# Optimization experiments

Measured on AMD Instinct MI355X. Metric: run time of the kernel, lower is better.

The kernel has to match this reference:

```python
import jax, jax.numpy as jnp
from jax import lax
import numpy as np

BN_EPS = 1e-5


def _dwconv3x3(x, w):
    # x: [B,C,H,W], w: [C,1,3,3] depthwise (groups == C)
    return lax.conv_general_dilated(
        x, w, window_strides=(1, 1), padding='SAME',
        dimension_numbers=('NCHW', 'OIHW', 'NCHW'),
        feature_group_count=x.shape[1])


def _bn_eval(x, g, b, m, v):
    s = g * lax.rsqrt(v + BN_EPS)            # [C]
    return x * s[None, :, None, None] + (b - m * s)[None, :, None, None]


def _maxpool2(x):
    return lax.reduce_window(x, -jnp.inf, lax.max,
                             (1, 1, 2, 2), (1, 1, 2, 2), 'VALID')


def setup_inputs() -> dict:
    key = jax.random.key(0)
    ks = jax.random.split(key, 8)
    B, Cin, H, W = 32, 128, 64, 64
    Hd = 256               # hidden_size
    K, Ck = 32, 8          # num categories, hidden_size // K
    sc = 0.05
    return {
        'v4_features': jax.random.normal(ks[0], (B, Cin, H, W), jnp.float32),
        'w1_dw': jax.random.normal(ks[1], (Cin, 1, 3, 3), jnp.float32) * sc,
        'w1_pw': jax.random.normal(ks[2], (Hd, Cin), jnp.float32) * sc,
        'bn1_g': jnp.ones((Hd,), jnp.float32),
        'bn1_b': jnp.zeros((Hd,), jnp.float32),
        'bn1_m': jnp.zeros((Hd,), jnp.float32),
        'bn1_v': jnp.ones((Hd,), jnp.float32),
        'w2_dw': jax.random.normal(ks[3], (Hd, 1, 3, 3), jnp.float32) * sc,
        'w2_pw': jax.random.normal(ks[4], (Hd, Hd), jnp.float32) * sc,
        'bn2_g': jnp.ones((Hd,), jnp.float32),
        'bn2_b': jnp.zeros((Hd,), jnp.float32),
        'bn2_m': jnp.zeros((Hd,), jnp.float32),
        'bn2_v': jnp.ones((Hd,), jnp.float32),
        'cat_w': jax.random.normal(ks[5], (K, Ck, Hd), jnp.float32) * sc,
        'emb_w': jax.random.normal(ks[6], (128, Hd), jnp.float32) * sc,
        'emb_b': jnp.zeros((128,), jnp.float32),
    }


def reference(v4_features, w1_dw, w1_pw, bn1_g, bn1_b, bn1_m, bn1_v,
              w2_dw, w2_pw, bn2_g, bn2_b, bn2_m, bn2_v,
              cat_w, emb_w, emb_b):
    # Block 1: depthwise 3x3 -> pointwise 1x1 -> BN -> ReLU -> maxpool2
    x = _dwconv3x3(v4_features, w1_dw)
    x = jnp.einsum('bchw,oc->bohw', x, w1_pw)
    x = _maxpool2(jax.nn.relu(_bn_eval(x, bn1_g, bn1_b, bn1_m, bn1_v)))
    # Block 2
    x = _dwconv3x3(x, w2_dw)
    x = jnp.einsum('bchw,oc->bohw', x, w2_pw)
    x = _maxpool2(jax.nn.relu(_bn_eval(x, bn2_g, bn2_b, bn2_m, bn2_v)))
    # All 32 category 1x1 convs fused into one batched contraction.
    # cat_spikes: [B, K, Ck, H', W'] (non-SNN branch returns raw features)
    cat_spikes = jnp.einsum('bchw,koc->bkohw', x, cat_w)
    cat_pooled = cat_spikes.mean(axis=(-2, -1))         # [B, K, Ck]
    category_activations = cat_pooled.mean(axis=-1)     # [B, K]
    pooled = x.mean(axis=(-2, -1))                      # [B, Hd]
    object_embedding = pooled @ emb_w.T + emb_b         # [B, 128]
    return cat_spikes, category_activations, object_embedding, x
```

## Files before the change

kernel.cpp:

```cpp
#include <hip/hip_runtime.h>

#define BN_EPS 1e-5f

typedef float f32x4 __attribute__((ext_vector_type(4)));
typedef short short8 __attribute__((ext_vector_type(8)));
typedef unsigned short u16;

__device__ __forceinline__ u16 f2bf(float f) {
    unsigned u = __builtin_bit_cast(unsigned, f);
    unsigned r = (u + 0x7FFFu + ((u >> 16) & 1u)) >> 16;
    return (u16)r;
}

#define SWZ(row) ((((row) & 7) ^ (((row) >> 3) & 7)) << 4)

template<int HW, int LOGW, int NPL, int IPP, int CMASK>
__global__ __launch_bounds__(256) void dw_shfl(
    const float* __restrict__ in, const float* __restrict__ wts,
    u16* __restrict__ out)
{
    const int t   = threadIdx.x;
    const int LPR = HW / 4;
    const int wq  = t & (LPR - 1);
    const int w0  = wq * 4;
    const int rin = t >> (LOGW - 2);

    for (int pl = 0; pl < NPL; ++pl) {
        const int plane = blockIdx.x * NPL + pl;
        const int c     = plane & CMASK;
        float wt[9];
#pragma unroll
        for (int i = 0; i < 9; ++i) wt[i] = wts[c * 9 + i];
        const float* ip = in  + (size_t)plane * (HW * HW);
        u16*         op = out + (size_t)plane * (HW * HW);

#pragma unroll
        for (int it = 0; it < IPP; ++it) {
            const int h = it * (1024 / HW) + rin;
            const float* rp = ip + h * HW + w0;
            const float4 zero4 = make_float4(0.f, 0.f, 0.f, 0.f);
            const float4 vc = *(const float4*)rp;
            const float4 vt = (h > 0)      ? *(const float4*)(rp - HW) : zero4;
            const float4 vb = (h < HW - 1) ? *(const float4*)(rp + HW) : zero4;

            float lc = __shfl_up(vc.w, 1),  rc = __shfl_down(vc.x, 1);
            float lt = __shfl_up(vt.w, 1),  rt = __shfl_down(vt.x, 1);
            float lb = __shfl_up(vb.w, 1),  rb = __shfl_down(vb.x, 1);
            if (wq == 0)       { lc = 0.f; lt = 0.f; lb = 0.f; }
            if (wq == LPR - 1) { rc = 0.f; rt = 0.f; rb = 0.f; }

            float o0 = 0.f, o1 = 0.f, o2 = 0.f, o3 = 0.f;
            o0 = fmaf(lt,   wt[0], fmaf(vt.x, wt[1], fmaf(vt.y, wt[2], o0)));
            o1 = fmaf(vt.x, wt[0], fmaf(vt.y, wt[1], fmaf(vt.z, wt[2], o1)));
            o2 = fmaf(vt.y, wt[0], fmaf(vt.z, wt[1], fmaf(vt.w, wt[2], o2)));
            o3 = fmaf(vt.z, wt[0], fmaf(vt.w, wt[1], fmaf(rt,   wt[2], o3)));
            o0 = fmaf(lc,   wt[3], fmaf(vc.x, wt[4], fmaf(vc.y, wt[5], o0)));
            o1 = fmaf(vc.x, wt[3], fmaf(vc.y, wt[4], fmaf(vc.z, wt[5], o1)));
            o2 = fmaf(vc.y, wt[3], fmaf(vc.z, wt[4], fmaf(vc.w, wt[5], o2)));
            o3 = fmaf(vc.z, wt[3], fmaf(vc.w, wt[4], fmaf(rc,   wt[5], o3)));
            o0 = fmaf(lb,   wt[6], fmaf(vb.x, wt[7], fmaf(vb.y, wt[8], o0)));
            o1 = fmaf(vb.x, wt[6], fmaf(vb.y, wt[7], fmaf(vb.z, wt[8], o1)));
            o2 = fmaf(vb.y, wt[6], fmaf(vb.z, wt[7], fmaf(vb.w, wt[8], o2)));
            o3 = fmaf(vb.z, wt[6], fmaf(vb.w, wt[7], fmaf(rb,   wt[8], o3)));

            ushort4 st;
            st.x = f2bf(o0); st.y = f2bf(o1); st.z = f2bf(o2); st.w = f2bf(o3);
            *(ushort4*)(op + h * HW + w0) = st;
        }
    }
}

__global__ __launch_bounds__(256) void pw1_mfma(
    const u16* __restrict__ t1b, const float* __restrict__ w,
    const float* __restrict__ bg, const float* __restrict__ bb,
    const float* __restrict__ bm, const float* __restrict__ bv,
    float* __restrict__ t2)
{
    __shared__ __align__(16) char smem[49664];
    float* sArr = (float*)(smem + 49152);
    float* tArr = (float*)(smem + 49408);
    float* Df   = (float*)smem;

    const int bid = blockIdx.x;
    const int o0  = ((bid >> 3) & 3) * 64;
    const int pxb = (bid >> 5) * 8 + (bid & 7);
    const int py  = pxb & 31;
    const int b   = pxb >> 5;
    const int p0  = py * 128;
    const int t   = threadIdx.x;

#pragma unroll
    for (int i = 0; i < 8; ++i) {
        const int li = i * 256 + t;
        const int ol = li >> 5;
        const int f4 = li & 31;
        const float4 wv = *(const float4*)(w + (size_t)(o0 + ol) * 128 + 4 * f4);
        ushort4 h;
        h.x = f2bf(wv.x); h.y = f2bf(wv.y); h.z = f2bf(wv.z); h.w = f2bf(wv.w);
        *(ushort4*)(smem + ((ol * 256 + f4 * 8) ^ SWZ(ol))) = h;
    }

    {
        const u16* xb = t1b + ((size_t)b * 128) * 4096 + p0;
        const int pg = t & 15, cg = t >> 4;
        short8 vin[8];
#pragma unroll
        for (int j = 0; j < 8; ++j)
            vin[j] = *(const short8*)(xb + (size_t)(8 * cg + j) * 4096 + 8 * pg);
#pragma unroll
        for (int k = 0; k < 8; ++k) {
            short8 ov;
            ov[0] = vin[0][k]; ov[1] = vin[1][k]; ov[2] = vin[2][k]; ov[3] = vin[3][k];
            ov[4] = vin[4][k]; ov[5] = vin[5][k]; ov[6] = vin[6][k]; ov[7] = vin[7][k];
            const int row = 8 * pg + k;
            *(short8*)(smem + 16384 + ((row * 256 + cg * 16) ^ SWZ(row))) = ov;
        }
    }

    if (t < 64) {
        const int o = o0 + t;
        const float s = bg[o] * rsqrtf(bv[o] + BN_EPS);
        sArr[t] = s;
        tArr[t] = bb[o] - bm[o] * s;
    }
    __syncthreads();

    const int lane = t & 63, wid = t >> 6;
    const int lr = lane & 15, lg = lane >> 4;
    const int wo = (wid >> 1) * 32;
    const int wp = (wid & 1) * 64;

    f32x4 acc[2][4];
#pragma unroll
    for (int m = 0; m < 2; ++m)
#pragma unroll
        for (int n = 0; n < 4; ++n) acc[m][n] = (f32x4){0.f, 0.f, 0.f, 0.f};

#pragma unroll
    for (int ks = 0; ks < 4; ++ks) {
        short8 af[2];
#pragma unroll
        for (int m = 0; m < 2; ++m) {
            const int rowm = wo + m * 16 + lr;
            af[m] = *(const short8*)(smem + ((rowm * 256 + ks * 64 + lg * 16) ^ SWZ(rowm)));
        }
#pragma unroll
        for (int n = 0; n < 4; ++n) {
            const int prow = wp + n * 16 + lr;
            const short8 bfv = *(const short8*)(smem + 16384 +
                ((prow * 256 + ks * 64 + lg * 16) ^ SWZ(prow)));
            acc[0][n] = __builtin_amdgcn_mfma_f32_16x16x32_bf16(af[0], bfv, acc[0][n], 0, 0, 0);
            acc[1][n] = __builtin_amdgcn_mfma_f32_16x16x32_bf16(af[1], bfv, acc[1][n], 0, 0, 0);
        }
    }
    __syncthreads();

    float sv[2][4], tv[2][4];
#pragma unroll
    for (int m = 0; m < 2; ++m)
#pragma unroll
        for (int j = 0; j < 4; ++j) {
            const int ol = wo + m * 16 + 4 * lg + j;
            sv[m][j] = sArr[ol];
            tv[m][j] = tArr[ol];
        }
#pragma unroll
    for (int m = 0; m < 2; ++m)
#pragma unroll
        for (int n = 0; n < 4; ++n)
#pragma unroll
            for (int j = 0; j < 4; ++j) {
                const int ol = wo + m * 16 + 4 * lg + j;
                const int pl = wp + n * 16 + lr;
                const float val = fmaf(acc[m][n][j], sv[m][j], tv[m][j]);
                Df[ol * 130 + pl] = fmaxf(val, 0.f);
            }
    __syncthreads();

#pragma unroll
    for (int i = 0; i < 8; ++i) {
        const int oi  = i * 256 + t;
        const int o   = oi >> 5;
        const int wpx = oi & 31;
        const float a0 = Df[o * 130 + 2 * wpx];
        const float a1 = Df[o * 130 + 2 * wpx + 1];
        const float b0 = Df[o * 130 + 64 + 2 * wpx];
        const float b1 = Df[o * 130 + 64 + 2 * wpx + 1];
        t2[(((size_t)(b * 256 + o0 + o)) * 32 + py) * 32 + wpx] =
            fmaxf(fmaxf(a0, a1), fmaxf(b0, b1));
    }
}

__global__ __launch_bounds__(256) void pw2_mfma(
    const u16* __restrict__ t3b, const float* __restrict__ w,
    const float* __restrict__ bg, const float* __restrict__ bb,
    const float* __restrict__ bm, const float* __restrict__ bv,
    float* __restrict__ xout)
{
    __shared__ __align__(16) char smem[49664];
    float* sArr = (float*)(smem + 49152);
    float* tArr = (float*)(smem + 49408);
    float* Df   = (float*)smem;

    const int bid = blockIdx.x;
    const int o0  = ((bid >> 3) & 3) * 64;
    const int pxb = (bid >> 5) * 8 + (bid & 7);
    const int px  = pxb & 7;
    const int b   = pxb >> 3;
    const int p0  = px * 128;
    const int t   = threadIdx.x;

    const int lane = t & 63, wid = t >> 6;
    const int lr = lane & 15, lg = lane >> 4;
    const int wo = (wid >> 1) * 32;
    const int wp = (wid & 1) * 64;

    f32x4 acc[2][4];
#pragma unroll
    for (int m = 0; m < 2; ++m)
#pragma unroll
        for (int n = 0; n < 4; ++n) acc[m][n] = (f32x4){0.f, 0.f, 0.f, 0.f};

#pragma unroll
    for (int ko = 0; ko < 2; ++ko) {
        if (ko) __syncthreads();

#pragma unroll
        for (int i = 0; i < 8; ++i) {
            const int li = i * 256 + t;
            const int ol = li >> 5;
            const int f4 = li & 31;
            const float4 wv = *(const float4*)(w + (size_t)(o0 + ol) * 256 + ko * 128 + 4 * f4);
            ushort4 h;
            h.x = f2bf(wv.x); h.y = f2bf(wv.y); h.z = f2bf(wv.z); h.w = f2bf(wv.w);
            *(ushort4*)(smem + ((ol * 256 + f4 * 8) ^ SWZ(ol))) = h;
        }

        {
            const u16* xb = t3b + ((size_t)b * 256 + ko * 128) * 1024 + p0;
            const int pg = t & 15, cg = t >> 4;
            short8 vin[8];
#pragma unroll
            for (int j = 0; j < 8; ++j)
                vin[j] = *(const short8*)(xb + (size_t)(8 * cg + j) * 1024 + 8 * pg);
#pragma unroll
            for (int k = 0; k < 8; ++k) {
                short8 ov;
                ov[0] = vin[0][k]; ov[1] = vin[1][k]; ov[2] = vin[2][k]; ov[3] = vin[3][k];
                ov[4] = vin[4][k]; ov[5] = vin[5][k]; ov[6] = vin[6][k]; ov[7] = vin[7][k];
                const int row = 8 * pg + k;
                *(short8*)(smem + 16384 + ((row * 256 + cg * 16) ^ SWZ(row))) = ov;
            }
        }

        if (ko == 0 && t < 64) {
            const int o = o0 + t;
            const float s = bg[o] * rsqrtf(bv[o] + BN_EPS);
            sArr[t] = s;
            tArr[t] = bb[o] - bm[o] * s;
        }
        __syncthreads();

#pragma unroll
        for (int ks = 0; ks < 4; ++ks) {
            short8 af[2];
#pragma unroll
            for (int m = 0; m < 2; ++m) {
                const int rowm = wo + m * 16 + lr;
                af[m] = *(const short8*)(smem + ((rowm * 256 + ks * 64 + lg * 16) ^ SWZ(rowm)));
            }
#pragma unroll
            for (int n = 0; n < 4; ++n) {
                const int prow = wp + n * 16 + lr;
                const short8 bfv = *(const short8*)(smem + 16384 +
                    ((prow * 256 + ks * 64 + lg * 16) ^ SWZ(prow)));
                acc[0][n] = __builtin_amdgcn_mfma_f32_16x16x32_bf16(af[0], bfv, acc[0][n], 0, 0, 0);
                acc[1][n] = __builtin_amdgcn_mfma_f32_16x16x32_bf16(af[1], bfv, acc[1][n], 0, 0, 0);
            }
        }
    }
    __syncthreads();

    float sv[2][4], tv[2][4];
#pragma unroll
    for (int m = 0; m < 2; ++m)
#pragma unroll
        for (int j = 0; j < 4; ++j) {
            const int ol = wo + m * 16 + 4 * lg + j;
            sv[m][j] = sArr[ol];
            tv[m][j] = tArr[ol];
        }
#pragma unroll
    for (int m = 0; m < 2; ++m)
#pragma unroll
        for (int n = 0; n < 4; ++n)
#pragma unroll
            for (int j = 0; j < 4; ++j) {
                const int ol = wo + m * 16 + 4 * lg + j;
                const int pl = wp + n * 16 + lr;
                const float val = fmaf(acc[m][n][j], sv[m][j], tv[m][j]);
                Df[ol * 130 + pl] = fmaxf(val, 0.f);
            }
    __syncthreads();

#pragma unroll
    for (int i = 0; i < 8; ++i) {
        const int oi = i * 256 + t;
        const int o  = oi >> 5;
        const int q  = oi & 31;
        const int prl = q >> 4;
        const int pc  = q & 15;
        const float a0 = Df[o * 130 + prl * 64 + 2 * pc];
        const float a1 = Df[o * 130 + prl * 64 + 2 * pc + 1];
        const float b0 = Df[o * 130 + prl * 64 + 32 + 2 * pc];
        const float b1 = Df[o * 130 + prl * 64 + 32 + 2 * pc + 1];
        xout[(((size_t)(b * 256 + o0 + o)) * 16 + 2 * px + prl) * 16 + pc] =
            fmaxf(fmaxf(a0, a1), fmaxf(b0, b1));
    }
}

__global__ __launch_bounds__(256) void cat_mfma(
    const float* __restrict__ x, const float* __restrict__ cw,
    float* __restrict__ spikes, float* __restrict__ catsum)
{
    __shared__ __align__(16) char smem[36864];
    __shared__ float cs[4][32];

    const int bid = blockIdx.x;
    const int b   = bid & 31;
    const int m0  = (bid >> 5) * 32;
    const int t   = threadIdx.x;

    const int lane = t & 63, wid = t >> 6;
    const int lr = lane & 15, lg = lane >> 4;
    const int wp = wid * 64;

    f32x4 acc[2][4];
#pragma unroll
    for (int m = 0; m < 2; ++m)
#pragma unroll
        for (int n = 0; n < 4; ++n) acc[m][n] = (f32x4){0.f, 0.f, 0.f, 0.f};

    const float* xb = x + (size_t)b * 65536;

#pragma unroll
    for (int ks = 0; ks < 4; ++ks) {
        if (ks) __syncthreads();

#pragma unroll
        for (int i = 0; i < 2; ++i) {
            const int li = i * 256 + t;
            const int ml = li >> 4;
            const int f4 = li & 15;
            const float4 wv = *(const float4*)(cw + (size_t)(m0 + ml) * 256 + ks * 64 + 4 * f4);
            ushort4 h;
            h.x = f2bf(wv.x); h.y = f2bf(wv.y); h.z = f2bf(wv.z); h.w = f2bf(wv.w);
            *(ushort4*)(smem + ((ml * 128 + f4 * 8) ^ SWZ(ml))) = h;
        }

#pragma unroll
        for (int i = 0; i < 4; ++i) {
            const int li = i * 256 + t;
            const int c4 = li >> 6;
            const int f4 = li & 63;
            float4 v0 = *(const float4*)(xb + (size_t)(ks * 64 + 4 * c4 + 0) * 256 + 4 * f4);
            float4 v1 = *(const float4*)(xb + (size_t)(ks * 64 + 4 * c4 + 1) * 256 + 4 * f4);
            float4 v2 = *(const float4*)(xb + (size_t)(ks * 64 + 4 * c4 + 2) * 256 + 4 * f4);
            float4 v3 = *(const float4*)(xb + (size_t)(ks * 64 + 4 * c4 + 3) * 256 + 4 * f4);
            ushort4 h0, h1, h2, h3;
            h0.x = f2bf(v0.x); h0.y = f2bf(v1.x); h0.z = f2bf(v2.x); h0.w = f2bf(v3.x);
            h1.x = f2bf(v0.y); h1.y = f2bf(v1.y); h1.z = f2bf(v2.y); h1.w = f2bf(v3.y);
            h2.x = f2bf(v0.z); h2.y = f2bf(v1.z); h2.z = f2bf(v2.z); h2.w = f2bf(v3.z);
            h3.x = f2bf(v0.w); h3.y = f2bf(v1.w); h3.z = f2bf(v2.w); h3.w = f2bf(v3.w);
            const int p_0 = 4 * f4;
            *(ushort4*)(smem + 4096 + (((p_0 + 0) * 128 + 8 * c4) ^ SWZ(p_0 + 0))) = h0;
            *(ushort4*)(smem + 4096 + (((p_0 + 1) * 128 + 8 * c4) ^ SWZ(p_0 + 1))) = h1;
            *(ushort4*)(smem + 4096 + (((p_0 + 2) * 128 + 8 * c4) ^ SWZ(p_0 + 2))) = h2;
            *(ushort4*)(smem + 4096 + (((p_0 + 3) * 128 + 8 * c4) ^ SWZ(p_0 + 3))) = h3;
        }
        __syncthreads();

#pragma unroll
        for (int kk = 0; kk < 2; ++kk) {
            short8 af[2];
#pragma unroll
            for (int m = 0; m < 2; ++m) {
                const int rowm = m * 16 + lr;
                af[m] = *(const short8*)(smem + ((rowm * 128 + kk * 64 + lg * 16) ^ SWZ(rowm)));
            }
#pragma unroll
            for (int n = 0; n < 4; ++n) {
                const int prow = wp + n * 16 + lr;
                const short8 bfv = *(const short8*)(smem + 4096 +
                    ((prow * 128 + kk * 64 + lg * 16) ^ SWZ(prow)));
                acc[0][n] = __builtin_amdgcn_mfma_f32_16x16x32_bf16(af[0], bfv, acc[0][n], 0, 0, 0);
                acc[1][n] = __builtin_amdgcn_mfma_f32_16x16x32_bf16(af[1], bfv, acc[1][n], 0, 0, 0);
            }
        }
    }

#pragma unroll
    for (int mi = 0; mi < 2; ++mi) {
#pragma unroll
        for (int j = 0; j < 4; ++j) {
            const int m = m0 + mi * 16 + 4 * lg + j;
#pragma unroll
            for (int n = 0; n < 4; ++n)
                spikes[((size_t)(b * 256 + m)) * 256 + wp + n * 16 + lr] = acc[mi][n][j];
            float s = acc[mi][0][j] + acc[mi][1][j] + acc[mi][2][j] + acc[mi][3][j];
            s += __shfl_xor(s, 1, 64);
            s += __shfl_xor(s, 2, 64);
            s += __shfl_xor(s, 4, 64);
            s += __shfl_xor(s, 8, 64);
            if (lr == 0) cs[wid][mi * 16 + 4 * lg + j] = s;
        }
    }
    __syncthreads();
    if (t < 32)
        catsum[b * 256 + m0 + t] = cs[0][t] + cs[1][t] + cs[2][t] + cs[3][t];
}

__global__ __launch_bounds__(256) void final_kernel(
    const float* __restrict__ x, const float* __restrict__ catsum,
    const float* __restrict__ embw, const float* __restrict__ embb,
    float* __restrict__ cat_act, float* __restrict__ emb)
{
    const int b = blockIdx.x;
    const int t = threadIdx.x;
    __shared__ __align__(16) float pooled[256];

    {
        const float4* src = (const float4*)(x + (size_t)b * 65536 + (size_t)t * 256);
        float s = 0.f;
#pragma unroll 8
        for (int i = 0; i < 64; ++i) {
            const float4 v = src[i];
            s += v.x + v.y + v.z + v.w;
        }
        pooled[t] = s * (1.0f / 256.0f);
    }
    __syncthreads();

    if (t < 128) {
        const float4* wr = (const float4*)(embw + (size_t)t * 256);
        float d = 0.f;
#pragma unroll 8
        for (int i = 0; i < 64; ++i) {
            const float4 wv = wr[i];
            const float4 pv = *(const float4*)&pooled[4 * i];
            d = fmaf(wv.x, pv.x, d);
            d = fmaf(wv.y, pv.y, d);
            d = fmaf(wv.z, pv.z, d);
            d = fmaf(wv.w, pv.w, d);
        }
        emb[b * 128 + t] = d + embb[t];
    } else if (t < 160) {
        const int k = t - 128;
        float s = 0.f;
#pragma unroll
        for (int o = 0; o < 8; ++o) s += catsum[b * 256 + k * 8 + o];
        cat_act[b * 32 + k] = s * (1.0f / 2048.0f);
    }
}

extern "C" void kernel_launch(void* const* d_in, const int* in_sizes, int n_in,
                              void* d_out, int out_size, void* d_ws, size_t ws_size,
                              hipStream_t stream) {
    const float* v4   = (const float*)d_in[0];
    const float* w1dw = (const float*)d_in[1];
    const float* w1pw = (const float*)d_in[2];
    const float* bn1g = (const float*)d_in[3];
    const float* bn1b = (const float*)d_in[4];
    const float* bn1m = (const float*)d_in[5];
    const float* bn1v = (const float*)d_in[6];
    const float* w2dw = (const float*)d_in[7];
    const float* w2pw = (const float*)d_in[8];
    const float* bn2g = (const float*)d_in[9];
    const float* bn2b = (const float*)d_in[10];
    const float* bn2m = (const float*)d_in[11];
    const float* bn2v = (const float*)d_in[12];
    const float* catw = (const float*)d_in[13];
    const float* embw = (const float*)d_in[14];
    const float* embb = (const float*)d_in[15];

    float* out        = (float*)d_out;
    float* cat_spikes = out;
    float* cat_act    = out + 2097152;
    float* emb        = out + 2098176;
    float* xout       = out + 2102272;

    char* ws = (char*)d_ws;
    u16*   t1b    = (u16*)ws;
    float* t2     = (float*)(ws + 33554432);
    float* catsum = (float*)(ws + 33554432 + 33554432);
    u16*   t3b    = (u16*)ws;

    dw_shfl<64, 6, 1, 4, 127><<<4096, 256, 0, stream>>>(v4, w1dw, t1b);
    pw1_mfma<<<4096, 256, 0, stream>>>(t1b, w1pw, bn1g, bn1b, bn1m, bn1v, t2);
    dw_shfl<32, 5, 4, 1, 255><<<2048, 256, 0, stream>>>(t2, w2dw, t3b);
    pw2_mfma<<<1024, 256, 0, stream>>>(t3b, w2pw, bn2g, bn2b, bn2m, bn2v, xout);
    cat_mfma<<<256, 256, 0, stream>>>(xout, catw, cat_spikes, catsum);
    final_kernel<<<32, 256, 0, stream>>>(xout, catsum, embw, embb, cat_act, emb);
}
```

Before: 111.1 us.

## Fuse block-1 depthwise and pointwise convs, store intermediates in bf16, pre-convert weights

Merges the first depthwise 3x3 conv with the pointwise MFMA GEMM, BN, ReLU and maxpool into one kernel. The depthwise output now goes to LDS instead of a 32MB bf16 round trip through global memory. The pooled block-1 output is stored as bf16 instead of fp32, and weights are converted to bf16 once by a prep kernel rather than in every block. The category-activation reduction moves into cat_mfma. This trades extra register pressure in the fused kernel (launch bounds 256,2) and more rounding to bf16 for less global traffic.

```diff
diff --git a/kernel.cpp b/kernel.cpp
--- a/kernel.cpp
+++ b/kernel.cpp
@@ -11,12 +11,157 @@
     unsigned r = (u + 0x7FFFu + ((u >> 16) & 1u)) >> 16;
     return (u16)r;
 }
+__device__ __forceinline__ float b2f(u16 h) {
+    return __builtin_bit_cast(float, (unsigned)h << 16);
+}
 
 #define SWZ(row) ((((row) & 7) ^ (((row) >> 3) & 7)) << 4)
 
+__global__ __launch_bounds__(256) void prep_bf16(
+    const float* __restrict__ w1, const float* __restrict__ w2,
+    const float* __restrict__ wc, u16* __restrict__ o1,
+    u16* __restrict__ o2, u16* __restrict__ oc)
+{
+    const int idx = blockIdx.x * 256 + threadIdx.x;
+    const float* src; u16* dst; int off;
+    if (idx < 8192)       { src = w1; dst = o1; off = idx; }
+    else if (idx < 24576) { src = w2; dst = o2; off = idx - 8192; }
+    else                  { src = wc; dst = oc; off = idx - 24576; }
+    const float4 v = *(const float4*)(src + 4 * (size_t)off);
+    ushort4 h;
+    h.x = f2bf(v.x); h.y = f2bf(v.y); h.z = f2bf(v.z); h.w = f2bf(v.w);
+    *(ushort4*)(dst + 4 * (size_t)off) = h;
+}
+
+__global__ __launch_bounds__(256, 2) void b1_fused(
+    const float* __restrict__ v4, const u16* __restrict__ wsW1,
+    const float* __restrict__ w1dw,
+    const float* __restrict__ bg, const float* __restrict__ bb,
+    const float* __restrict__ bm, const float* __restrict__ bv,
+    u16* __restrict__ t2b)
+{
+    __shared__ __align__(16) char smem[34816];
+    float* sArr = (float*)(smem + 32768);
+    float* tArr = (float*)(smem + 33792);
+
+    const int bid = blockIdx.x;
+    const int b   = bid >> 5;
+    const int py  = bid & 31;
+    const int t   = threadIdx.x;
+    const int c    = t & 127;
+    const int half = t >> 7;
+    const int R    = 2 * py + half;
+
+    {
+        const float s = bg[t] * rsqrtf(bv[t] + BN_EPS);
+        sArr[t] = s;
+        tArr[t] = bb[t] - bm[t] * s;
+    }
+
+    float wt[9];
+#pragma unroll
+    for (int i = 0; i < 9; ++i) wt[i] = w1dw[c * 9 + i];
+
+    {
+        const float* vp = v4 + ((size_t)(b * 128 + c)) * 4096;
+        float prevw[3] = {0.f, 0.f, 0.f};
+#pragma unroll
+        for (int ch = 0; ch < 4; ++ch) {
+            const int x0 = ch * 16;
+            float in[3][18];
+#pragma unroll
+            for (int j = 0; j < 3; ++j) {
+                const int Rj = R - 1 + j;
+                const bool ok = (Rj >= 0) && (Rj < 64);
+                const float* rp = vp + Rj * 64 + x0;
+                float4 q0, q1, q2, q3;
+                if (ok) {
+                    q0 = *(const float4*)(rp);
+                    q1 = *(const float4*)(rp + 4);
+                    q2 = *(const float4*)(rp + 8);
+                    q3 = *(const float4*)(rp + 12);
+                } else {
+                    q0 = q1 = q2 = q3 = make_float4(0.f, 0.f, 0.f, 0.f);
+                }
+                in[j][0]  = prevw[j];
+                in[j][1]  = q0.x; in[j][2]  = q0.y; in[j][3]  = q0.z; in[j][4]  = q0.w;
+                in[j][5]  = q1.x; in[j][6]  = q1.y; in[j][7]  = q1.z; in[j][8]  = q1.w;
+                in[j][9]  = q2.x; in[j][10] = q2.y; in[j][11] = q2.z; in[j][12] = q2.w;
+                in[j][13] = q3.x; in[j][14] = q3.y; in[j][15] = q3.z; in[j][16] = q3.w;
+                in[j][17] = (ok && ch < 3) ? rp[16] : 0.f;
+                prevw[j] = q3.w;
+            }
+#pragma unroll
+            for (int x = 0; x < 16; ++x) {
+                float s = 0.f;
+#pragma unroll
+                for (int j = 0; j < 3; ++j)
+                    s = fmaf(in[j][x], wt[3 * j],
+                        fmaf(in[j][x + 1], wt[3 * j + 1],
+                        fmaf(in[j][x + 2], wt[3 * j + 2], s)));
+                const int p = half * 64 + x0 + x;
+                *(u16*)(smem + ((p * 256 + 2 * c) ^ SWZ(p))) = f2bf(s);
+            }
+        }
+    }
+    __syncthreads();
+
+    const int lane = t & 63, wid = t >> 6;
+    const int lr = lane & 15, lg = lane >> 4;
+    const int wo = wid * 64;
+
+    f32x4 acc[4][8];
+#pragma unroll
+    for (int m = 0; m < 4; ++m)
+#pragma unroll
+        for (int n = 0; n < 8; ++n) acc[m][n] = (f32x4){0.f, 0.f, 0.f, 0.f};
+
+    const u16* wbase = wsW1 + (size_t)(wo + lr) * 128 + lg * 8;
+#pragma unroll
+    for (int ks = 0; ks < 4; ++ks) {
+        short8 af[4];
+#pragma unroll
+        for (int m = 0; m < 4; ++m)
+            af[m] = *(const short8*)(wbase + m * 16 * 128 + ks * 32);
+#pragma unroll
+        for (int n = 0; n < 8; ++n) {
+            const int prow = n * 16 + lr;
+            const short8 bfv = *(const short8*)(smem +
+                ((prow * 256 + ks * 64 + lg * 16) ^ SWZ(prow)));
+#pragma unroll
+            for (int m = 0; m < 4; ++m)
+                acc[m][n] = __builtin_amdgcn_mfma_f32_16x16x32_bf16(af[m], bfv, acc[m][n], 0, 0, 0);
+        }
+    }
+
+    u16* outb = t2b + ((size_t)(b * 256) * 32 + py) * 32;
+#pragma unroll
+    for (int m = 0; m < 4; ++m) {
+#pragma unroll
+        for (int j = 0; j < 4; ++j) {
+            const int o = wo + m * 16 + 4 * lg + j;
+            const float s = sArr[o], tt = tArr[o];
+#pragma unroll
+            for (int n = 0; n < 4; ++n) {
+                const float a0 = fmaxf(fmaf(acc[m][n][j],     s, tt), 0.f);
+                const float a1 = fmaxf(fmaf(acc[m][n + 4][j], s, tt), 0.f);
+                const float vm = fmaxf(a0, a1);
+                const float hm = fmaxf(vm, __shfl_xor(vm, 1));
+                const unsigned p2 = (unsigned)f2bf(hm) |
+                                    ((unsigned)f2bf(__shfl_xor(hm, 2)) << 16);
+                const unsigned hi = __shfl_xor(p2, 4);
+                if ((lr & 7) == 0) {
+                    uint2 w2v; w2v.x = p2; w2v.y = hi;
+                    *(uint2*)(outb + (size_t)o * 1024 + n * 8 + (lr >> 1)) = w2v;
+                }
+            }
+        }
+    }
+}
+
 template<int HW, int LOGW, int NPL, int IPP, int CMASK>
-__global__ __launch_bounds__(256) void dw_shfl(
-    const float* __restrict__ in, const float* __restrict__ wts,
+__global__ __launch_bounds__(256) void dw_shfl_bf(
+    const u16* __restrict__ in, const float* __restrict__ wts,
     u16* __restrict__ out)
 {
     const int t   = threadIdx.x;
@@ -31,17 +176,26 @@
         float wt[9];
 #pragma unroll
         for (int i = 0; i < 9; ++i) wt[i] = wts[c * 9 + i];
-        const float* ip = in  + (size_t)plane * (HW * HW);
-        u16*         op = out + (size_t)plane * (HW * HW);
+        const u16* ip = in  + (size_t)plane * (HW * HW);
+        u16*       op = out + (size_t)plane * (HW * HW);
 
 #pragma unroll
         for (int it = 0; it < IPP; ++it) {
             const int h = it * (1024 / HW) + rin;
-            const float* rp = ip + h * HW + w0;
-            const float4 zero4 = make_float4(0.f, 0.f, 0.f, 0.f);
-            const float4 vc = *(const float4*)rp;
-            const float4 vt = (h > 0)      ? *(const float4*)(rp - HW) : zero4;
-            const float4 vb = (h < HW - 1) ? *(const float4*)(rp + HW) : zero4;
+            const u16* rp = ip + h * HW + w0;
+            float4 vc, vt, vb;
+            {
+                const ushort4 hcv = *(const ushort4*)rp;
+                vc = make_float4(b2f(hcv.x), b2f(hcv.y), b2f(hcv.z), b2f(hcv.w));
+            }
+            if (h > 0) {
+                const ushort4 htv = *(const ushort4*)(rp - HW);
+                vt = make_float4(b2f(htv.x), b2f(htv.y), b2f(htv.z), b2f(htv.w));
+            } else vt = make_float4(0.f, 0.f, 0.f, 0.f);
+            if (h < HW - 1) {
+                const ushort4 hbv = *(const ushort4*)(rp + HW);
+                vb = make_float4(b2f(hbv.x), b2f(hbv.y), b2f(hbv.z), b2f(hbv.w));
+            } else vb = make_float4(0.f, 0.f, 0.f, 0.f);
 
             float lc = __shfl_up(vc.w, 1),  rc = __shfl_down(vc.x, 1);
             float lt = __shfl_up(vt.w, 1),  rt = __shfl_down(vt.x, 1);
@@ -70,129 +224,8 @@
     }
 }
 
-__global__ __launch_bounds__(256) void pw1_mfma(
-    const u16* __restrict__ t1b, const float* __restrict__ w,
-    const float* __restrict__ bg, const float* __restrict__ bb,
-    const float* __restrict__ bm, const float* __restrict__ bv,
-    float* __restrict__ t2)
-{
-    __shared__ __align__(16) char smem[49664];
-    float* sArr = (float*)(smem + 49152);
-    float* tArr = (float*)(smem + 49408);
-    float* Df   = (float*)smem;
-
-    const int bid = blockIdx.x;
-    const int o0  = ((bid >> 3) & 3) * 64;
-    const int pxb = (bid >> 5) * 8 + (bid & 7);
-    const int py  = pxb & 31;
-    const int b   = pxb >> 5;
-    const int p0  = py * 128;
-    const int t   = threadIdx.x;
-
-#pragma unroll
-    for (int i = 0; i < 8; ++i) {
-        const int li = i * 256 + t;
-        const int ol = li >> 5;
-        const int f4 = li & 31;
-        const float4 wv = *(const float4*)(w + (size_t)(o0 + ol) * 128 + 4 * f4);
-        ushort4 h;
-        h.x = f2bf(wv.x); h.y = f2bf(wv.y); h.z = f2bf(wv.z); h.w = f2bf(wv.w);
-        *(ushort4*)(smem + ((ol * 256 + f4 * 8) ^ SWZ(ol))) = h;
-    }
-
-    {
-        const u16* xb = t1b + ((size_t)b * 128) * 4096 + p0;
-        const int pg = t & 15, cg = t >> 4;
-        short8 vin[8];
-#pragma unroll
-        for (int j = 0; j < 8; ++j)
-            vin[j] = *(const short8*)(xb + (size_t)(8 * cg + j) * 4096 + 8 * pg);
-#pragma unroll
-        for (int k = 0; k < 8; ++k) {
-            short8 ov;
-            ov[0] = vin[0][k]; ov[1] = vin[1][k]; ov[2] = vin[2][k]; ov[3] = vin[3][k];
-            ov[4] = vin[4][k]; ov[5] = vin[5][k]; ov[6] = vin[6][k]; ov[7] = vin[7][k];
-            const int row = 8 * pg + k;
-            *(short8*)(smem + 16384 + ((row * 256 + cg * 16) ^ SWZ(row))) = ov;
-        }
-    }
-
-    if (t < 64) {
-        const int o = o0 + t;
-        const float s = bg[o] * rsqrtf(bv[o] + BN_EPS);
-        sArr[t] = s;
-        tArr[t] = bb[o] - bm[o] * s;
-    }
-    __syncthreads();
-
-    const int lane = t & 63, wid = t >> 6;
-    const int lr = lane & 15, lg = lane >> 4;
-    const int wo = (wid >> 1) * 32;
-    const int wp = (wid & 1) * 64;
-
-    f32x4 acc[2][4];
-#pragma unroll
-    for (int m = 0; m < 2; ++m)
-#pragma unroll
-        for (int n = 0; n < 4; ++n) acc[m][n] = (f32x4){0.f, 0.f, 0.f, 0.f};
-
-#pragma unroll
-    for (int ks = 0; ks < 4; ++ks) {
-        short8 af[2];
-#pragma unroll
-        for (int m = 0; m < 2; ++m) {
-            const int rowm = wo + m * 16 + lr;
-            af[m] = *(const short8*)(smem + ((rowm * 256 + ks * 64 + lg * 16) ^ SWZ(rowm)));
-        }
-#pragma unroll
-        for (int n = 0; n < 4; ++n) {
-            const int prow = wp + n * 16 + lr;
-            const short8 bfv = *(const short8*)(smem + 16384 +
-                ((prow * 256 + ks * 64 + lg * 16) ^ SWZ(prow)));
-            acc[0][n] = __builtin_amdgcn_mfma_f32_16x16x32_bf16(af[0], bfv, acc[0][n], 0, 0, 0);
-            acc[1][n] = __builtin_amdgcn_mfma_f32_16x16x32_bf16(af[1], bfv, acc[1][n], 0, 0, 0);
-        }
-    }
-    __syncthreads();
-
-    float sv[2][4], tv[2][4];
-#pragma unroll
-    for (int m = 0; m < 2; ++m)
-#pragma unroll
-        for (int j = 0; j < 4; ++j) {
-            const int ol = wo + m * 16 + 4 * lg + j;
-            sv[m][j] = sArr[ol];
-            tv[m][j] = tArr[ol];
-        }
-#pragma unroll
-    for (int m = 0; m < 2; ++m)
-#pragma unroll
-        for (int n = 0; n < 4; ++n)
-#pragma unroll
-            for (int j = 0; j < 4; ++j) {
-                const int ol = wo + m * 16 + 4 * lg + j;
-                const int pl = wp + n * 16 + lr;
-                const float val = fmaf(acc[m][n][j], sv[m][j], tv[m][j]);
-                Df[ol * 130 + pl] = fmaxf(val, 0.f);
-            }
-    __syncthreads();
-
-#pragma unroll
-    for (int i = 0; i < 8; ++i) {
-        const int oi  = i * 256 + t;
-        const int o   = oi >> 5;
-        const int wpx = oi & 31;
-        const float a0 = Df[o * 130 + 2 * wpx];
-        const float a1 = Df[o * 130 + 2 * wpx + 1];
-        const float b0 = Df[o * 130 + 64 + 2 * wpx];
-        const float b1 = Df[o * 130 + 64 + 2 * wpx + 1];
-        t2[(((size_t)(b * 256 + o0 + o)) * 32 + py) * 32 + wpx] =
-            fmaxf(fmaxf(a0, a1), fmaxf(b0, b1));
-    }
-}
-
 __global__ __launch_bounds__(256) void pw2_mfma(
-    const u16* __restrict__ t3b, const float* __restrict__ w,
+    const u16* __restrict__ t3b, const u16* __restrict__ wsW2,
     const float* __restrict__ bg, const float* __restrict__ bb,
     const float* __restrict__ bm, const float* __restrict__ bv,
     float* __restrict__ xout)
@@ -226,14 +259,12 @@
         if (ko) __syncthreads();
 
 #pragma unroll
-        for (int i = 0; i < 8; ++i) {
+        for (int i = 0; i < 4; ++i) {
             const int li = i * 256 + t;
-            const int ol = li >> 5;
-            const int f4 = li & 31;
-            const float4 wv = *(const float4*)(w + (size_t)(o0 + ol) * 256 + ko * 128 + 4 * f4);
-            ushort4 h;
-            h.x = f2bf(wv.x); h.y = f2bf(wv.y); h.z = f2bf(wv.z); h.w = f2bf(wv.w);
-            *(ushort4*)(smem + ((ol * 256 + f4 * 8) ^ SWZ(ol))) = h;
+            const int ol = li >> 4;
+            const int f8 = li & 15;
+            const short8 wv = *(const short8*)(wsW2 + (size_t)(o0 + ol) * 256 + ko * 128 + 8 * f8);
+            *(short8*)(smem + ((ol * 256 + f8 * 16) ^ SWZ(ol))) = wv;
         }
 
         {
@@ -320,11 +351,12 @@
 }
 
 __global__ __launch_bounds__(256) void cat_mfma(
-    const float* __restrict__ x, const float* __restrict__ cw,
-    float* __restrict__ spikes, float* __restrict__ catsum)
+    const float* __restrict__ x, const u16* __restrict__ wsWc,
+    float* __restrict__ spikes, float* __restrict__ cat_act)
 {
     __shared__ __align__(16) char smem[36864];
     __shared__ float cs[4][32];
+    __shared__ float msum[32];
 
     const int bid = blockIdx.x;
     const int b   = bid & 31;
@@ -347,15 +379,11 @@
     for (int ks = 0; ks < 4; ++ks) {
         if (ks) __syncthreads();
 
-#pragma unroll
-        for (int i = 0; i < 2; ++i) {
-            const int li = i * 256 + t;
-            const int ml = li >> 4;
-            const int f4 = li & 15;
-            const float4 wv = *(const float4*)(cw + (size_t)(m0 + ml) * 256 + ks * 64 + 4 * f4);
-            ushort4 h;
-            h.x = f2bf(wv.x); h.y = f2bf(wv.y); h.z = f2bf(wv.z); h.w = f2bf(wv.w);
-            *(ushort4*)(smem + ((ml * 128 + f4 * 8) ^ SWZ(ml))) = h;
+        if (t < 256) {
+            const int ol = t >> 3;
+            const int f8 = t & 7;
+            const short8 wv = *(const short8*)(wsWc + (size_t)(m0 + ol) * 256 + ks * 64 + 8 * f8);
+            *(short8*)(smem + ((ol * 128 + f8 * 16) ^ SWZ(ol))) = wv;
         }
 
 #pragma unroll
@@ -416,14 +444,20 @@
         }
     }
     __syncthreads();
-    if (t < 32)
-        catsum[b * 256 + m0 + t] = cs[0][t] + cs[1][t] + cs[2][t] + cs[3][t];
+    if (t < 32) msum[t] = cs[0][t] + cs[1][t] + cs[2][t] + cs[3][t];
+    __syncthreads();
+    if (t < 4) {
+        float s = 0.f;
+#pragma unroll
+        for (int o = 0; o < 8; ++o) s += msum[t * 8 + o];
+        cat_act[b * 32 + (m0 >> 3) + t] = s * (1.0f / 2048.0f);
+    }
 }
 
 __global__ __launch_bounds__(256) void final_kernel(
-    const float* __restrict__ x, const float* __restrict__ catsum,
+    const float* __restrict__ x,
     const float* __restrict__ embw, const float* __restrict__ embb,
-    float* __restrict__ cat_act, float* __restrict__ emb)
+    float* __restrict__ emb)
 {
     const int b = blockIdx.x;
     const int t = threadIdx.x;
@@ -454,12 +488,6 @@
             d = fmaf(wv.w, pv.w, d);
         }
         emb[b * 128 + t] = d + embb[t];
-    } else if (t < 160) {
-        const int k = t - 128;
-        float s = 0.f;
-#pragma unroll
-        for (int o = 0; o < 8; ++o) s += catsum[b * 256 + k * 8 + o];
-        cat_act[b * 32 + k] = s * (1.0f / 2048.0f);
     }
 }
 
@@ -490,15 +518,16 @@
     float* xout       = out + 2102272;
 
     char* ws = (char*)d_ws;
-    u16*   t1b    = (u16*)ws;
-    float* t2     = (float*)(ws + 33554432);
-    float* catsum = (float*)(ws + 33554432 + 33554432);
-    u16*   t3b    = (u16*)ws;
-
-    dw_shfl<64, 6, 1, 4, 127><<<4096, 256, 0, stream>>>(v4, w1dw, t1b);
-    pw1_mfma<<<4096, 256, 0, stream>>>(t1b, w1pw, bn1g, bn1b, bn1m, bn1v, t2);
-    dw_shfl<32, 5, 4, 1, 255><<<2048, 256, 0, stream>>>(t2, w2dw, t3b);
-    pw2_mfma<<<1024, 256, 0, stream>>>(t3b, w2pw, bn2g, bn2b, bn2m, bn2v, xout);
-    cat_mfma<<<256, 256, 0, stream>>>(xout, catw, cat_spikes, catsum);
-    final_kernel<<<32, 256, 0, stream>>>(xout, catsum, embw, embb, cat_act, emb);
-}
+    u16* wsW1 = (u16*)ws;
+    u16* wsW2 = (u16*)(ws + 65536);
+    u16* wsWc = (u16*)(ws + 196608);
+    u16* t2b  = (u16*)(ws + 327680);
+    u16* t3b  = (u16*)(ws + 327680 + 16777216);
+
+    prep_bf16<<<160, 256, 0, stream>>>(w1pw, w2pw, catw, wsW1, wsW2, wsWc);
+    b1_fused<<<1024, 256, 0, stream>>>(v4, wsW1, w1dw, bn1g, bn1b, bn1m, bn1v, t2b);
+    dw_shfl_bf<32, 5, 4, 1, 255><<<2048, 256, 0, stream>>>(t2b, w2dw, t3b);
+    pw2_mfma<<<1024, 256, 0, stream>>>(t3b, wsW2, bn2g, bn2b, bn2m, bn2v, xout);
+    cat_mfma<<<256, 256, 0, stream>>>(xout, wsWc, cat_spikes, cat_act);
+    final_kernel<<<32, 256, 0, stream>>>(xout, embw, embb, emb);
+}
```

Measured after the change: 114.5 us. +3.1%, slower.
